# Kernel tuning notes

Hardware: AMD Instinct MI355X
Metric: run time of the kernel (lower is better)

## Reference

```python
import jax, jax.numpy as jnp
import numpy as np

H = 200  # hidden size
I = 129  # input features (n_fft bins)


def _lstm_layer(x, w_ih, w_hh, b_ih, b_hh):
    """PyTorch-convention LSTM. x: [B,T,I]; w_ih: [4H,I]; w_hh: [4H,H].
    Gate order i, f, g, o. Returns hidden sequence [B,T,H]."""
    B, T, _ = x.shape
    Hh = w_hh.shape[1]
    # Precompute input contribution for all timesteps (one big GEMM).
    xg = jnp.einsum('bti,gi->btg', x, w_ih) + b_ih + b_hh  # [B,T,4H]
    xg = jnp.swapaxes(xg, 0, 1)  # [T,B,4H] time-major for scan

    def step(carry, xg_t):
        h, c = carry
        g = xg_t + h @ w_hh.T  # [B,4H]
        i, f, gg, o = jnp.split(g, 4, axis=-1)
        i = jax.nn.sigmoid(i)
        f = jax.nn.sigmoid(f)
        gg = jnp.tanh(gg)
        o = jax.nn.sigmoid(o)
        c = f * c + i * gg
        h = o * jnp.tanh(c)
        return (h, c), h

    h0 = jnp.zeros((B, Hh), x.dtype)
    (_, _), hs = jax.lax.scan(step, (h0, h0), xg)
    return jnp.swapaxes(hs, 0, 1)  # [B,T,H]


def setup_inputs() -> dict:
    key = jax.random.key(0)
    ks = jax.random.split(key, 16)
    B, T = 256, 600
    s1 = 1.0 / np.sqrt(H)
    u = lambda k, shape: jax.random.uniform(k, shape, jnp.float32, -s1, s1)
    return {
        'x': jax.random.normal(ks[0], (B, I, T), jnp.float32),
        'w_ih1': u(ks[1], (4 * H, I)),
        'w_hh1': u(ks[2], (4 * H, H)),
        'b_ih1': u(ks[3], (4 * H,)),
        'b_hh1': u(ks[4], (4 * H,)),
        'w_ih2': u(ks[5], (4 * H, H)),
        'w_hh2': u(ks[6], (4 * H, H)),
        'b_ih2': u(ks[7], (4 * H,)),
        'b_hh2': u(ks[8], (4 * H,)),
        'fc1_w': u(ks[9], (I, H)),
        'fc1_b': u(ks[10], (I,)),
        'fc2_w': u(ks[11], (I, I)),
        'fc2_b': u(ks[12], (I,)),
    }


def reference(x, w_ih1, w_hh1, b_ih1, b_hh1,
              w_ih2, w_hh2, b_ih2, b_hh2,
              fc1_w, fc1_b, fc2_w, fc2_b):
    lstm_in = jnp.transpose(x, (0, 2, 1))  # [B,T,129]
    h1 = _lstm_layer(lstm_in, w_ih1, w_hh1, b_ih1, b_hh1)  # [B,T,200]
    h2 = _lstm_layer(h1, w_ih2, w_hh2, b_ih2, b_hh2)       # [B,T,200]
    y = jax.nn.relu(h2 @ fc1_w.T + fc1_b)                  # [B,T,129]
    y = jax.nn.sigmoid(y @ fc2_w.T + fc2_b)                # [B,T,129]
    return jnp.transpose(y, (0, 2, 1))                     # [B,129,T]
```

## Files before the change

### kernel.cpp

```cpp
#include <hip/hip_runtime.h>

typedef unsigned short u16;
typedef short short8 __attribute__((ext_vector_type(8)));
typedef float f32x4 __attribute__((ext_vector_type(4)));
typedef unsigned short u16x4 __attribute__((ext_vector_type(4)));

#define B_  256
#define T_  600
#define TC_ 75
#define HID 200
#define G4  800
#define HSTR 232
#define HROW (B_ * HID)

__device__ __forceinline__ float bf2f(u16 u) {
  union { unsigned int i; float f; } v; v.i = ((unsigned int)u) << 16; return v.f;
}
__device__ __forceinline__ u16 f2bf(float f) {
  union { float f; unsigned int i; } v; v.f = f;
  unsigned int r = v.i + 0x7FFFu + ((v.i >> 16) & 1u);
  return (u16)(r >> 16);
}
__device__ __forceinline__ float sigm(float x) {
  float e = __expf(-x);
  return __builtin_amdgcn_rcpf(1.f + e);
}

#define BARRIER_LGKM() asm volatile("s_waitcnt lgkmcnt(0)\n\ts_barrier" ::: "memory")
#define BARRIER_ONLY() asm volatile("s_barrier" ::: "memory")

__global__ __launch_bounds__(256) void padperm_k(const float* __restrict__ src,
                                                 u16* __restrict__ dst,
                                                 int rows, int srows, int scols,
                                                 int dcols, int perm) {
  int idx = blockIdx.x * 256 + threadIdx.x;
  if (idx >= rows * dcols) return;
  int r = idx / dcols, c = idx - r * dcols;
  int sr = perm ? ((r & 3) * 200 + (r >> 2)) : r;
  dst[idx] = (r < srows && c < scols) ? f2bf(src[(size_t)sr * scols + c]) : (u16)0;
}

__global__ __launch_bounds__(256) void transpose_k(const float* __restrict__ x,
                                                   u16* __restrict__ xTq, int t0) {
  __shared__ u16 tile[129 * 65];
  const int b = blockIdx.y;
  const int tt0 = blockIdx.x * 64;
  const int tid = threadIdx.x;
  for (int idx = tid; idx < 129 * 64; idx += 256) {
    int i = idx >> 6, tt = idx & 63;
    int t = t0 + tt0 + tt;
    tile[i * 65 + tt] = (tt0 + tt < TC_ && t < T_)
        ? f2bf(x[((size_t)b * 129 + i) * T_ + t]) : (u16)0;
  }
  __syncthreads();
  for (int idx = tid; idx < 64 * 160; idx += 256) {
    int tt = idx / 160, i = idx - tt * 160;
    if (tt0 + tt < TC_)
      xTq[((size_t)b * TC_ + tt0 + tt) * 160 + i] = (i < 129) ? tile[i * 65 + tt] : (u16)0;
  }
}

template<int ASRC, int LDK, int NSRC, int NSTORE, int BPERM, int ACT, int OUTM, int AMAP>
__global__ __launch_bounds__(256, 2) void gemm_k(
    const u16* __restrict__ A, const u16* __restrict__ W,
    const float* __restrict__ B1, const float* __restrict__ B2,
    void* __restrict__ outv, int ldout, int t0) {
  constexpr int NCH = LDK / 8;
  constexpr int KT = LDK / 32;
  __shared__ u16 la[128 * LDK];
  __shared__ float lbias[128];
  const int tid = threadIdx.x;
  const int mb = blockIdx.x, nb = blockIdx.y;

  for (int idx = tid; idx < 128 * NCH; idx += 256) {
    int row = idx / NCH, c = idx - row * NCH;
    int m = mb * 128 + row;
    size_t arow;
    if (AMAP == 1) {
      int b = m / TC_; int tt = m - b * TC_;
      arow = (size_t)b * T_ + t0 + tt;
    } else if (AMAP == 2) {
      int b = m / TC_; int tt = m - b * TC_;
      arow = (size_t)tt * B_ + b;
    } else if (AMAP == 3) {
      int b = m / T_; int tt = m - b * T_;
      arow = (size_t)tt * B_ + b;
    } else {
      arow = (size_t)m;
    }
    short8 v = (short8)0;
    if (8 * c + 8 <= ASRC)
      v = *(const short8*)(A + arow * ASRC + 8 * c);
    *(short8*)(la + row * LDK + 8 * c) = v;
  }
  if (tid < 128) {
    int p = nb * 128 + tid;
    float bv = 0.f;
    if (p < NSRC) {
      int orig = BPERM ? ((p & 3) * 200 + (p >> 2)) : p;
      bv = B1[orig];
      if (BPERM) bv += B2[orig];
    }
    lbias[tid] = bv;
  }
  __syncthreads();

  const int w = tid >> 6, l = tid & 63;
  const int quad = l >> 4, l15 = l & 15;
  const int mq = (w >> 1) * 64, nq = (w & 1) * 64;

  const u16* wrow[4];
#pragma unroll
  for (int nt = 0; nt < 4; ++nt) {
    int p = nb * 128 + nq + nt * 16 + l15;
    wrow[nt] = W + (size_t)((p < NSRC) ? p : 0) * LDK;
  }

  f32x4 acc[4][4];
#pragma unroll
  for (int i = 0; i < 4; ++i)
#pragma unroll
    for (int j = 0; j < 4; ++j) acc[i][j] = (f32x4)0.f;

#pragma unroll
  for (int kt = 0; kt < KT; ++kt) {
    const int k0 = kt * 32 + quad * 8;
    short8 bf[4];
#pragma unroll
    for (int nt = 0; nt < 4; ++nt) bf[nt] = *(const short8*)(wrow[nt] + k0);
    short8 af[4];
#pragma unroll
    for (int mt = 0; mt < 4; ++mt)
      af[mt] = *(const short8*)(la + (mq + mt * 16 + l15) * LDK + k0);
#pragma unroll
    for (int mt = 0; mt < 4; ++mt)
#pragma unroll
      for (int nt = 0; nt < 4; ++nt)
        acc[mt][nt] = __builtin_amdgcn_mfma_f32_16x16x32_bf16(af[mt], bf[nt],
                                                              acc[mt][nt], 0, 0, 0);
  }

#pragma unroll
  for (int mt = 0; mt < 4; ++mt) {
#pragma unroll
    for (int nt = 0; nt < 4; ++nt) {
#pragma unroll
      for (int r = 0; r < 4; ++r) {
        int rowl = mq + mt * 16 + quad * 4 + r;
        int coln = nq + nt * 16 + l15;
        int pg = nb * 128 + coln;
        if (pg < NSTORE) {
          float v = (pg < NSRC) ? (acc[mt][nt][r] + lbias[coln]) : 0.f;
          if (ACT == 1) v = fmaxf(v, 0.f);
          if (ACT == 2) v = sigm(v);
          size_t m = (size_t)mb * 128 + rowl;
          if (OUTM == 0) {
            ((u16*)outv)[m * (size_t)ldout + pg] = f2bf(v);
          } else {
            int b = (int)(m / T_);
            int t = (int)(m - (size_t)b * T_);
            ((float*)outv)[((size_t)b * 129 + pg) * T_ + t] = v;
          }
        }
      }
    }
  }
}

__device__ __forceinline__ void rec_body(const u16* __restrict__ xg,
                                         const u16* __restrict__ whh,
                                         u16* __restrict__ hout,
                                         const u16* __restrict__ hprev,
                                         float* __restrict__ cst, int has_prev,
                                         int blk, char* smem) {
  u16* hb  = (u16*)smem;
  u16* w45 = (u16*)(smem + 7424);
  u16* w6  = (u16*)(smem + 109824);

  const int tid = threadIdx.x;
  const int w = tid >> 6, l = tid & 63;
  const int quad = l >> 4, l15 = l & 15;
  const int b0 = blk * 16;
  const bool four = (w < 2);

  short8 wreg[4][4];
#pragma unroll
  for (int s = 0; s < 4; ++s) {
    const bool act = (s < 3) || four;
    int tile = w + 16 * s;
    int p = tile * 16 + l15;
    int orig = (p & 3) * 200 + (p >> 2);
    const u16* wb = whh + (size_t)orig * HID;
#pragma unroll
    for (int kk = 0; kk < 4; ++kk)
      wreg[s][kk] = act ? *(const short8*)(wb + kk * 32 + quad * 8) : (short8)0;
    if (act) {
#pragma unroll
      for (int j = 0; j < 2; ++j)
        *(short8*)(w45 + (tile * 2 + j) * 512 + l * 8) =
            *(const short8*)(wb + (4 + j) * 32 + quad * 8);
      if (quad == 0)
        *(short8*)(w6 + tile * 128 + l15 * 8) = *(const short8*)(wb + 192);
    }
  }
  if (tid < 512) {
    int r = tid >> 5, cc = tid & 31;
    hb[r * HSTR + 200 + cc] = 0;
  }

  float c[4]; u16 hreg[4];
#pragma unroll
  for (int s = 0; s < 4; ++s) { c[s] = 0.f; hreg[s] = 0; }
  float* cstp = cst + (size_t)(b0 + l15) * HID;
  if (has_prev) {
#pragma unroll
    for (int s = 0; s < 3; ++s) {
      int unit = (w + 16 * s) * 4 + quad;
      hreg[s] = hprev[(size_t)(b0 + l15) * HID + unit];
      c[s] = cstp[unit];
    }
    if (four) {
      int unit = (w + 48) * 4 + quad;
      hreg[3] = hprev[(size_t)(b0 + l15) * HID + unit];
      c[3] = cstp[unit];
    }
  }

  const u16* xptr = xg + (size_t)(b0 + l15) * TC_ * G4 + w * 16 + quad * 4;
  u16x4 xv[4];
#pragma unroll
  for (int s = 0; s < 3; ++s) xv[s] = *(const u16x4*)(xptr + s * 256);
  xv[3] = four ? *(const u16x4*)(xptr + 768) : (u16x4)0;

  __syncthreads();

  for (int t = 0; t < TC_; ++t) {
#pragma unroll
    for (int s = 0; s < 3; ++s)
      hb[l15 * HSTR + (w + 16 * s) * 4 + quad] = hreg[s];
    if (four)
      hb[l15 * HSTR + (w + 48) * 4 + quad] = hreg[3];
    BARRIER_LGKM();

    if (t > 0 && tid < 400) {
      int row = tid / 25, seg = tid - row * 25;
      *(short8*)(hout + (size_t)(t - 1) * HROW + (size_t)(b0 + row) * HID + seg * 8) =
          *(const short8*)(hb + row * HSTR + seg * 8);
    }

    f32x4 acc[4];
#pragma unroll
    for (int s = 0; s < 4; ++s) acc[s] = (f32x4)0.f;

#pragma unroll
    for (int kk = 0; kk < 4; ++kk) {
      short8 hf = *(const short8*)(hb + l15 * HSTR + kk * 32 + quad * 8);
      acc[0] = __builtin_amdgcn_mfma_f32_16x16x32_bf16(wreg[0][kk], hf, acc[0], 0, 0, 0);
      acc[1] = __builtin_amdgcn_mfma_f32_16x16x32_bf16(wreg[1][kk], hf, acc[1], 0, 0, 0);
      acc[2] = __builtin_amdgcn_mfma_f32_16x16x32_bf16(wreg[2][kk], hf, acc[2], 0, 0, 0);
      if (four)
        acc[3] = __builtin_amdgcn_mfma_f32_16x16x32_bf16(wreg[3][kk], hf, acc[3], 0, 0, 0);
    }
#pragma unroll
    for (int j = 0; j < 2; ++j) {
      short8 hf = *(const short8*)(hb + l15 * HSTR + (4 + j) * 32 + quad * 8);
#pragma unroll
      for (int s = 0; s < 3; ++s) {
        short8 wz = *(const short8*)(w45 + ((w + 16 * s) * 2 + j) * 512 + l * 8);
        acc[s] = __builtin_amdgcn_mfma_f32_16x16x32_bf16(wz, hf, acc[s], 0, 0, 0);
      }
      if (four) {
        short8 wz = *(const short8*)(w45 + ((w + 48) * 2 + j) * 512 + l * 8);
        acc[3] = __builtin_amdgcn_mfma_f32_16x16x32_bf16(wz, hf, acc[3], 0, 0, 0);
      }
    }
    {
      short8 hf = *(const short8*)(hb + l15 * HSTR + 192 + quad * 8);
#pragma unroll
      for (int s = 0; s < 3; ++s) {
        short8 wz = (short8)0;
        if (quad == 0)
          wz = *(const short8*)(w6 + (w + 16 * s) * 128 + l15 * 8);
        acc[s] = __builtin_amdgcn_mfma_f32_16x16x32_bf16(wz, hf, acc[s], 0, 0, 0);
      }
      if (four) {
        short8 wz = (short8)0;
        if (quad == 0)
          wz = *(const short8*)(w6 + (w + 48) * 128 + l15 * 8);
        acc[3] = __builtin_amdgcn_mfma_f32_16x16x32_bf16(wz, hf, acc[3], 0, 0, 0);
      }
    }

#pragma unroll
    for (int s = 0; s < 4; ++s) {
      if (s == 3 && !four) break;
      float vi = acc[s][0] + bf2f(xv[s][0]);
      float vf = acc[s][1] + bf2f(xv[s][1]);
      float vg = acc[s][2] + bf2f(xv[s][2]);
      float vo = acc[s][3] + bf2f(xv[s][3]);
      float iv = sigm(vi);
      float fv = sigm(vf);
      float gv = 2.f * sigm(2.f * vg) - 1.f;
      float ov = sigm(vo);
      float cn = fv * c[s] + iv * gv;
      c[s] = cn;
      float th = 2.f * sigm(2.f * cn) - 1.f;
      hreg[s] = f2bf(ov * th);
    }

    if (t + 1 < TC_) {
      const u16* xp = xptr + (size_t)(t + 1) * G4;
#pragma unroll
      for (int s = 0; s < 3; ++s) xv[s] = *(const u16x4*)(xp + s * 256);
      if (four) xv[3] = *(const u16x4*)(xp + 768);
    }
    BARRIER_ONLY();
  }

#pragma unroll
  for (int s = 0; s < 3; ++s) {
    int unit = (w + 16 * s) * 4 + quad;
    hout[(size_t)(TC_ - 1) * HROW + (size_t)(b0 + l15) * HID + unit] = hreg[s];
    cstp[unit] = c[s];
  }
  if (four) {
    int unit = (w + 48) * 4 + quad;
    hout[(size_t)(TC_ - 1) * HROW + (size_t)(b0 + l15) * HID + unit] = hreg[3];
    cstp[unit] = c[3];
  }
}

__global__ __launch_bounds__(1024) void recp_k(
    const u16* __restrict__ xgA, const u16* __restrict__ whhA,
    u16* __restrict__ hA, const u16* __restrict__ hpA, int prevA,
    float* __restrict__ cstA,
    const u16* __restrict__ xgB, const u16* __restrict__ whhB,
    u16* __restrict__ hB, const u16* __restrict__ hpB, int prevB,
    float* __restrict__ cstB, int nA) {
  __shared__ __align__(16) char smem[122624];
  const int bb = blockIdx.x;
  if (bb < nA) rec_body(xgA, whhA, hA, hpA, cstA, prevA, bb, smem);
  else         rec_body(xgB, whhB, hB, hpB, cstB, prevB, bb - nA, smem);
}

extern "C" void kernel_launch(void* const* d_in, const int* in_sizes, int n_in,
                              void* d_out, int out_size, void* d_ws, size_t ws_size,
                              hipStream_t stream) {
  (void)in_sizes; (void)n_in; (void)out_size; (void)ws_size;
  const float* x     = (const float*)d_in[0];
  const float* w_ih1 = (const float*)d_in[1];
  const float* w_hh1 = (const float*)d_in[2];
  const float* b_ih1 = (const float*)d_in[3];
  const float* b_hh1 = (const float*)d_in[4];
  const float* w_ih2 = (const float*)d_in[5];
  const float* w_hh2 = (const float*)d_in[6];
  const float* b_ih2 = (const float*)d_in[7];
  const float* b_hh2 = (const float*)d_in[8];
  const float* fc1_w = (const float*)d_in[9];
  const float* fc1_b = (const float*)d_in[10];
  const float* fc2_w = (const float*)d_in[11];
  const float* fc2_b = (const float*)d_in[12];
  float* out = (float*)d_out;

  char* ws = (char*)d_ws;
  u16*   xgA   = (u16*)(ws);
  u16*   xgB   = (u16*)(ws + 30720000LL);
  u16*   h2    = (u16*)(ws + 61440000LL);
  u16*   h1c0  = (u16*)(ws + 122880000LL);
  u16*   h1c1  = (u16*)(ws + 130560000LL);
  u16*   xTq   = (u16*)(ws + 138240000LL);
  float* cst1  = (float*)(ws + 144384000LL);
  float* cst2  = (float*)(ws + 144588800LL);
  u16*   wp1   = (u16*)(ws + 144793600LL);
  u16*   wp2   = (u16*)(ws + 145049600LL);
  u16*   fc1p  = (u16*)(ws + 145408000LL);
  u16*   fc2p  = (u16*)(ws + 145465792LL);
  u16*   whh1c = (u16*)(ws + 145507072LL);
  u16*   whh2c = (u16*)(ws + 145827072LL);
  u16*   y1    = (u16*)(ws);

  u16* h1c[2] = {h1c0, h1c1};

  padperm_k<<<(800 * 160 + 255) / 256, 256, 0, stream>>>(w_ih1, wp1, 800, 800, 129, 160, 1);
  padperm_k<<<(800 * 224 + 255) / 256, 256, 0, stream>>>(w_ih2, wp2, 800, 800, 200, 224, 1);
  padperm_k<<<(129 * 224 + 255) / 256, 256, 0, stream>>>(fc1_w, fc1p, 129, 129, 200, 224, 0);
  padperm_k<<<(129 * 160 + 255) / 256, 256, 0, stream>>>(fc2_w, fc2p, 129, 129, 129, 160, 0);
  padperm_k<<<(800 * 200 + 255) / 256, 256, 0, stream>>>(w_hh1, whh1c, 800, 800, 200, 200, 0);
  padperm_k<<<(800 * 200 + 255) / 256, 256, 0, stream>>>(w_hh2, whh2c, 800, 800, 200, 200, 0);

  transpose_k<<<dim3(2, 256), 256, 0, stream>>>(x, xTq, 0);
  gemm_k<160, 160, 800, 800, 1, 0, 0, 0>
      <<<dim3(150, 7), 256, 0, stream>>>(xTq, wp1, b_ih1, b_hh1, xgA, 800, 0);
  recp_k<<<dim3(16), 1024, 0, stream>>>(xgA, whh1c, h1c0, h1c0, 0, cst1,
                                        xgA, whh1c, h1c0, h1c0, 0, cst1, 16);

  for (int i = 0; i < 7; ++i) {
    const int tB = i * TC_;
    transpose_k<<<dim3(2, 256), 256, 0, stream>>>(x, xTq, (i + 1) * TC_);
    gemm_k<160, 160, 800, 800, 1, 0, 0, 0>
        <<<dim3(150, 7), 256, 0, stream>>>(xTq, wp1, b_ih1, b_hh1, xgA, 800, 0);
    gemm_k<200, 224, 800, 800, 1, 0, 0, 2>
        <<<dim3(150, 7), 256, 0, stream>>>(h1c[i & 1], wp2, b_ih2, b_hh2, xgB, 800, 0);
    recp_k<<<dim3(32), 1024, 0, stream>>>(
        xgA, whh1c, h1c[(i + 1) & 1], h1c[i & 1] + (size_t)(TC_ - 1) * HROW, 1, cst1,
        xgB, whh2c, h2 + (size_t)tB * HROW,
        (i >= 1) ? (h2 + (size_t)(tB - 1) * HROW) : h2, (i >= 1) ? 1 : 0, cst2, 16);
  }

  gemm_k<200, 224, 800, 800, 1, 0, 0, 2>
      <<<dim3(150, 7), 256, 0, stream>>>(h1c[7 & 1], wp2, b_ih2, b_hh2, xgB, 800, 0);
  recp_k<<<dim3(16), 1024, 0, stream>>>(
      xgA, whh1c, h1c0, h1c0, 0, cst1,
      xgB, whh2c, h2 + (size_t)(7 * TC_) * HROW, h2 + (size_t)(7 * TC_ - 1) * HROW, 1,
      cst2, 0);

  gemm_k<200, 224, 129, 144, 0, 1, 0, 3>
      <<<dim3(1200, 2), 256, 0, stream>>>(h2, fc1p, fc1_b, fc1_b, y1, 144, 0);
  gemm_k<144, 160, 129, 129, 0, 2, 1, 0>
      <<<dim3(1200, 2), 256, 0, stream>>>(y1, fc2p, fc2_b, fc2_b, out, 0, 0);
}
```

Baseline: 2.550 ms.

## Fuse layer-1 input GEMM and transpose into recurrent kernel launch

Adds a fused kernel whose blocks, selected by block index, run the two LSTM recurrences, the next chunk's layer-1 input-projection GEMM, and the transpose of the chunk after that. Buffers for xg1 and the transposed input are double-buffered so these stages can overlap. The intent is to fill the idle CUs left by the 32-block recurrent launch with independent work and to cut the number of kernel launches. The cost is extra workspace and the risk that the co-scheduled blocks contend with the latency-critical recurrent blocks.

```diff
diff --git a/kernel.cpp b/kernel.cpp
--- a/kernel.cpp
+++ b/kernel.cpp
@@ -76,10 +76,7 @@
     int row = idx / NCH, c = idx - row * NCH;
     int m = mb * 128 + row;
     size_t arow;
-    if (AMAP == 1) {
-      int b = m / TC_; int tt = m - b * TC_;
-      arow = (size_t)b * T_ + t0 + tt;
-    } else if (AMAP == 2) {
+    if (AMAP == 2) {
       int b = m / TC_; int tt = m - b * TC_;
       arow = (size_t)tt * B_ + b;
     } else if (AMAP == 3) {
@@ -330,17 +327,134 @@
   }
 }
 
-__global__ __launch_bounds__(1024) void recp_k(
+__device__ __forceinline__ void gemm1_body(const u16* __restrict__ A,
+                                           const u16* __restrict__ W,
+                                           const float* __restrict__ B1,
+                                           const float* __restrict__ B2,
+                                           u16* __restrict__ out, int bb,
+                                           char* smem) {
+  u16* la = (u16*)smem;
+  float* lbias = (float*)(smem + 40960);
+  const int tid = threadIdx.x;
+  const int mpair = bb >> 1, nb = bb & 1;
+
+  if (tid < 512) {
+    int p = nb * 512 + tid;
+    float bv = 0.f;
+    if (p < 800) { int orig = (p & 3) * 200 + (p >> 2); bv = B1[orig] + B2[orig]; }
+    lbias[tid] = bv;
+  }
+
+  const int w = tid >> 6, l = tid & 63;
+  const int quad = l >> 4, l15 = l & 15;
+  const int mq = (w >> 3) * 64, nq = (w & 7) * 64;
+
+  const u16* wrow[4];
+#pragma unroll
+  for (int nt = 0; nt < 4; ++nt) {
+    int p = nb * 512 + nq + nt * 16 + l15;
+    wrow[nt] = W + (size_t)((p < 800) ? p : 0) * 160;
+  }
+
+  for (int mi = 0; mi < 2; ++mi) {
+    const int mb = mpair * 2 + mi;
+    if (mi) __syncthreads();
+    for (int idx = tid; idx < 128 * 20; idx += 1024) {
+      int row = idx / 20, cc = idx - row * 20;
+      *(short8*)(la + row * 160 + 8 * cc) =
+          *(const short8*)(A + (size_t)(mb * 128 + row) * 160 + 8 * cc);
+    }
+    __syncthreads();
+
+    f32x4 acc[4][4];
+#pragma unroll
+    for (int i = 0; i < 4; ++i)
+#pragma unroll
+      for (int j = 0; j < 4; ++j) acc[i][j] = (f32x4)0.f;
+
+#pragma unroll
+    for (int kt = 0; kt < 5; ++kt) {
+      const int k0 = kt * 32 + quad * 8;
+      short8 bf[4];
+#pragma unroll
+      for (int nt = 0; nt < 4; ++nt) bf[nt] = *(const short8*)(wrow[nt] + k0);
+      short8 af[4];
+#pragma unroll
+      for (int mt = 0; mt < 4; ++mt)
+        af[mt] = *(const short8*)(la + (mq + mt * 16 + l15) * 160 + k0);
+#pragma unroll
+      for (int mt = 0; mt < 4; ++mt)
+#pragma unroll
+        for (int nt = 0; nt < 4; ++nt)
+          acc[mt][nt] = __builtin_amdgcn_mfma_f32_16x16x32_bf16(af[mt], bf[nt],
+                                                                acc[mt][nt], 0, 0, 0);
+    }
+
+#pragma unroll
+    for (int mt = 0; mt < 4; ++mt) {
+#pragma unroll
+      for (int nt = 0; nt < 4; ++nt) {
+#pragma unroll
+        for (int r = 0; r < 4; ++r) {
+          int rowl = mq + mt * 16 + quad * 4 + r;
+          int coln = nq + nt * 16 + l15;
+          int pg = nb * 512 + coln;
+          if (pg < 800) {
+            float v = acc[mt][nt][r] + lbias[coln];
+            out[(size_t)(mb * 128 + rowl) * 800 + pg] = f2bf(v);
+          }
+        }
+      }
+    }
+  }
+}
+
+__device__ __forceinline__ void transpose_body(const float* __restrict__ x,
+                                               u16* __restrict__ xTq, int t0,
+                                               int bb, char* smem) {
+  const int tid = threadIdx.x;
+  const int sl = tid >> 8, stid = tid & 255;
+  u16* tile = (u16*)(smem + sl * 16800);
+  const int b = bb * 4 + sl;
+  for (int half = 0; half < 2; ++half) {
+    const int tt0 = half * 64;
+    __syncthreads();
+    for (int idx = stid; idx < 129 * 64; idx += 256) {
+      int i = idx >> 6, tt = idx & 63;
+      int t = t0 + tt0 + tt;
+      tile[i * 65 + tt] = (tt0 + tt < TC_ && t < T_)
+          ? f2bf(x[((size_t)b * 129 + i) * T_ + t]) : (u16)0;
+    }
+    __syncthreads();
+    for (int idx = stid; idx < 64 * 160; idx += 256) {
+      int tt = idx / 160, i = idx - tt * 160;
+      if (tt0 + tt < TC_)
+        xTq[((size_t)b * TC_ + tt0 + tt) * 160 + i] = (i < 129) ? tile[i * 65 + tt] : (u16)0;
+    }
+  }
+}
+
+__global__ __launch_bounds__(1024) void fused_k(
     const u16* __restrict__ xgA, const u16* __restrict__ whhA,
     u16* __restrict__ hA, const u16* __restrict__ hpA, int prevA,
     float* __restrict__ cstA,
     const u16* __restrict__ xgB, const u16* __restrict__ whhB,
     u16* __restrict__ hB, const u16* __restrict__ hpB, int prevB,
-    float* __restrict__ cstB, int nA) {
+    float* __restrict__ cstB,
+    const u16* __restrict__ gA, const u16* __restrict__ gW,
+    const float* __restrict__ gB1, const float* __restrict__ gB2,
+    u16* __restrict__ gOut,
+    const float* __restrict__ tX, u16* __restrict__ tOut, int tT0,
+    int nA, int nB, int nG, int nT) {
   __shared__ __align__(16) char smem[122624];
-  const int bb = blockIdx.x;
-  if (bb < nA) rec_body(xgA, whhA, hA, hpA, cstA, prevA, bb, smem);
-  else         rec_body(xgB, whhB, hB, hpB, cstB, prevB, bb - nA, smem);
+  int bb = blockIdx.x;
+  if (bb < nA) { rec_body(xgA, whhA, hA, hpA, cstA, prevA, bb, smem); return; }
+  bb -= nA;
+  if (bb < nB) { rec_body(xgB, whhB, hB, hpB, cstB, prevB, bb, smem); return; }
+  bb -= nB;
+  if (bb < nG) { gemm1_body(gA, gW, gB1, gB2, gOut, bb, smem); return; }
+  bb -= nG;
+  if (bb < nT) transpose_body(tX, tOut, tT0, bb, smem);
 }
 
 extern "C" void kernel_launch(void* const* d_in, const int* in_sizes, int n_in,
@@ -363,22 +477,26 @@
   float* out = (float*)d_out;
 
   char* ws = (char*)d_ws;
-  u16*   xgA   = (u16*)(ws);
-  u16*   xgB   = (u16*)(ws + 30720000LL);
-  u16*   h2    = (u16*)(ws + 61440000LL);
-  u16*   h1c0  = (u16*)(ws + 122880000LL);
-  u16*   h1c1  = (u16*)(ws + 130560000LL);
-  u16*   xTq   = (u16*)(ws + 138240000LL);
-  float* cst1  = (float*)(ws + 144384000LL);
-  float* cst2  = (float*)(ws + 144588800LL);
-  u16*   wp1   = (u16*)(ws + 144793600LL);
-  u16*   wp2   = (u16*)(ws + 145049600LL);
-  u16*   fc1p  = (u16*)(ws + 145408000LL);
-  u16*   fc2p  = (u16*)(ws + 145465792LL);
-  u16*   whh1c = (u16*)(ws + 145507072LL);
-  u16*   whh2c = (u16*)(ws + 145827072LL);
+  u16*   xg1a  = (u16*)(ws);
+  u16*   xg1b  = (u16*)(ws + 30720000LL);
+  u16*   xg2   = (u16*)(ws + 61440000LL);
+  u16*   h2    = (u16*)(ws + 92160000LL);
+  u16*   h1c0  = (u16*)(ws + 153600000LL);
+  u16*   h1c1  = (u16*)(ws + 161280000LL);
+  u16*   xTq0  = (u16*)(ws + 168960000LL);
+  u16*   xTq1  = (u16*)(ws + 175104000LL);
+  float* cst1  = (float*)(ws + 181248000LL);
+  float* cst2  = (float*)(ws + 181452800LL);
+  u16*   wp1   = (u16*)(ws + 181657600LL);
+  u16*   wp2   = (u16*)(ws + 181913600LL);
+  u16*   fc1p  = (u16*)(ws + 182272000LL);
+  u16*   fc2p  = (u16*)(ws + 182329792LL);
+  u16*   whh1c = (u16*)(ws + 182371072LL);
+  u16*   whh2c = (u16*)(ws + 182691072LL);
   u16*   y1    = (u16*)(ws);
 
+  u16* xg1[2] = {xg1a, xg1b};
+  u16* xTq[2] = {xTq0, xTq1};
   u16* h1c[2] = {h1c0, h1c1};
 
   padperm_k<<<(800 * 160 + 255) / 256, 256, 0, stream>>>(w_ih1, wp1, 800, 800, 129, 160, 1);
@@ -388,31 +506,30 @@
   padperm_k<<<(800 * 200 + 255) / 256, 256, 0, stream>>>(w_hh1, whh1c, 800, 800, 200, 200, 0);
   padperm_k<<<(800 * 200 + 255) / 256, 256, 0, stream>>>(w_hh2, whh2c, 800, 800, 200, 200, 0);
 
-  transpose_k<<<dim3(2, 256), 256, 0, stream>>>(x, xTq, 0);
+  transpose_k<<<dim3(2, 256), 256, 0, stream>>>(x, xTq0, 0);
+  transpose_k<<<dim3(2, 256), 256, 0, stream>>>(x, xTq1, TC_);
   gemm_k<160, 160, 800, 800, 1, 0, 0, 0>
-      <<<dim3(150, 7), 256, 0, stream>>>(xTq, wp1, b_ih1, b_hh1, xgA, 800, 0);
-  recp_k<<<dim3(16), 1024, 0, stream>>>(xgA, whh1c, h1c0, h1c0, 0, cst1,
-                                        xgA, whh1c, h1c0, h1c0, 0, cst1, 16);
-
-  for (int i = 0; i < 7; ++i) {
-    const int tB = i * TC_;
-    transpose_k<<<dim3(2, 256), 256, 0, stream>>>(x, xTq, (i + 1) * TC_);
-    gemm_k<160, 160, 800, 800, 1, 0, 0, 0>
-        <<<dim3(150, 7), 256, 0, stream>>>(xTq, wp1, b_ih1, b_hh1, xgA, 800, 0);
-    gemm_k<200, 224, 800, 800, 1, 0, 0, 2>
-        <<<dim3(150, 7), 256, 0, stream>>>(h1c[i & 1], wp2, b_ih2, b_hh2, xgB, 800, 0);
-    recp_k<<<dim3(32), 1024, 0, stream>>>(
-        xgA, whh1c, h1c[(i + 1) & 1], h1c[i & 1] + (size_t)(TC_ - 1) * HROW, 1, cst1,
-        xgB, whh2c, h2 + (size_t)tB * HROW,
-        (i >= 1) ? (h2 + (size_t)(tB - 1) * HROW) : h2, (i >= 1) ? 1 : 0, cst2, 16);
-  }
-
-  gemm_k<200, 224, 800, 800, 1, 0, 0, 2>
-      <<<dim3(150, 7), 256, 0, stream>>>(h1c[7 & 1], wp2, b_ih2, b_hh2, xgB, 800, 0);
-  recp_k<<<dim3(16), 1024, 0, stream>>>(
-      xgA, whh1c, h1c0, h1c0, 0, cst1,
-      xgB, whh2c, h2 + (size_t)(7 * TC_) * HROW, h2 + (size_t)(7 * TC_ - 1) * HROW, 1,
-      cst2, 0);
+      <<<dim3(150, 7), 256, 0, stream>>>(xTq0, wp1, b_ih1, b_hh1, xg1a, 800, 0);
+
+  for (int i = 0; i <= 8; ++i) {
+    const int nA = (i <= 7) ? 16 : 0;
+    const int nB = (i >= 1) ? 16 : 0;
+    const int nG = (i <= 6) ? 150 : 0;
+    const int nT = (i <= 5) ? 64 : 0;
+    const int j = (i >= 1) ? (i - 1) : 0;
+    fused_k<<<dim3(nA + nB + nG + nT), 1024, 0, stream>>>(
+        xg1[i & 1], whh1c, h1c[i & 1],
+        (i >= 1) ? (h1c[(i - 1) & 1] + (size_t)(TC_ - 1) * HROW) : h1c[0], (i >= 1) ? 1 : 0,
+        cst1,
+        xg2, whh2c, h2 + (size_t)j * TC_ * HROW,
+        (j >= 1) ? (h2 + ((size_t)j * TC_ - 1) * HROW) : h2, (j >= 1) ? 1 : 0, cst2,
+        xTq[(i + 1) & 1], wp1, b_ih1, b_hh1, xg1[(i + 1) & 1],
+        x, xTq[i & 1], (i + 2) * TC_,
+        nA, nB, nG, nT);
+    if (i <= 7)
+      gemm_k<200, 224, 800, 800, 1, 0, 0, 2>
+          <<<dim3(150, 7), 256, 0, stream>>>(h1c[i & 1], wp2, b_ih2, b_hh2, xg2, 800, 0);
+  }
 
   gemm_k<200, 224, 129, 144, 0, 1, 0, 3>
       <<<dim3(1200, 2), 256, 0, stream>>>(h2, fc1p, fc1_b, fc1_b, y1, 144, 0);
```

After: 2.292 ms. 10.1% less time.
